# Kernel optimization log

Hardware: AMD Instinct MI355X
Metric: run time of the kernel (lower is better)

The kernel has to match this reference:

```python
import jax, jax.numpy as jnp
import numpy as np
from jax import lax

B, L, R = 128, 256, 36
D_TXT, D_IMG, D_SOC = 768, 2048, 10
EPS = 0.05 ** 2        # geomloss blur=0.05, p=2 -> epsilon = blur^p
N_ITERS = 20           # fixed log-domain Sinkhorn iterations
GAMMA = 0.01


def _pcost(x, y):
    # x: [B,n,d], y: [B,m,d] -> C_ij = ||x_i - y_j||^2 / 2 (geomloss p=2 cost)
    xx = jnp.sum(x * x, -1)[:, :, None]
    yy = jnp.sum(y * y, -1)[:, None, :]
    xy = jnp.einsum('bnd,bmd->bnm', x, y)
    return 0.5 * (xx + yy - 2.0 * xy)


def _sinkhorn_cost(C, loga, logb, eps, n_iters):
    # Log-domain Sinkhorn; masked points carry loga/logb = -inf (zero weight).
    f = jnp.zeros(loga.shape, C.dtype)
    g = jnp.zeros(logb.shape, C.dtype)

    def body(fg, _):
        f, g = fg
        g = -eps * jax.nn.logsumexp(loga[:, :, None] + (f[:, :, None] - C) / eps, axis=1)
        f = -eps * jax.nn.logsumexp(logb[:, None, :] + (g[:, None, :] - C) / eps, axis=2)
        return (f, g), None

    (f, g), _ = lax.scan(body, (f, g), None, length=n_iters)
    a = jnp.exp(loga)  # exp(-inf) = 0 for masked entries
    b = jnp.exp(logb)
    return jnp.sum(a * f, -1) + jnp.sum(b * g, -1)  # <a,f> + <b,g>


def _forward(txt_global, txt_region, img_global, img_region, social, attn_mask,
             W_stat, b_stat, W_gt, b_gt, W_gi, b_gi, W_rt, b_rt, W_ri, b_ri,
             W_m1, b_m1, W_m2, b_m2):
    relu = jax.nn.relu
    soc = relu(social @ W_stat + b_stat)                            # [B,100]
    tg = relu(jnp.concatenate([txt_global, soc], axis=1) @ W_gt + b_gt)  # [B,200]
    ig = relu(img_global @ W_gi + b_gi)                              # [B,200]
    h = relu((tg + ig) @ W_m1 + b_m1)
    mix_pred = h @ W_m2 + b_m2                                       # [B,2]

    tr = relu(txt_region @ W_rt + b_rt)                              # [B,L,50]
    ir = relu(img_region @ W_ri + b_ri)                              # [B,R,50]

    Bn, _, _ = tr.shape
    Rn = ir.shape[1]
    mask = attn_mask > 0
    n_words = jnp.sum(attn_mask, axis=-1).astype(tr.dtype)          # [B]
    loga = jnp.where(mask, -jnp.log(n_words)[:, None], -jnp.inf)    # uniform over valid tokens
    logb = jnp.full((Bn, Rn), -jnp.log(float(Rn)), tr.dtype)        # uniform over regions

    # Debiased Sinkhorn divergence (geomloss SamplesLoss default debias=True):
    Sxy = _sinkhorn_cost(_pcost(tr, ir), loga, logb, EPS, N_ITERS)
    Sxx = _sinkhorn_cost(_pcost(tr, tr), loga, loga, EPS, N_ITERS)
    Syy = _sinkhorn_cost(_pcost(ir, ir), logb, logb, EPS, N_ITERS)
    w_dis = Sxy - 0.5 * (Sxx + Syy)                                  # [B]

    w_pred = jnp.stack([1.0 - GAMMA * w_dis, GAMMA * w_dis], axis=1)  # [B,2]
    logit = jax.nn.softmax(jnp.maximum(mix_pred, w_pred), axis=1)
    return logit


def setup_inputs() -> dict:
    key = jax.random.key(0)
    ks = jax.random.split(key, 24)
    init = lambda k, s: (jax.random.normal(k, s) * 0.02).astype(jnp.float32)
    lengths = jax.random.randint(ks[0], (B,), 16, L + 1)             # ragged lengths
    attn_mask = (jnp.arange(L)[None, :] < lengths[:, None]).astype(jnp.int32)
    return {
        'txt_global': jax.random.normal(ks[1], (B, D_TXT), jnp.float32),
        'txt_region': jax.random.normal(ks[2], (B, L, D_TXT), jnp.float32),
        'img_global': jax.random.normal(ks[3], (B, D_IMG), jnp.float32),
        'img_region': jax.random.normal(ks[4], (B, R, D_IMG), jnp.float32),
        'social': jax.random.normal(ks[5], (B, D_SOC), jnp.float32),
        'attn_mask': attn_mask,
        'W_stat': init(ks[6], (D_SOC, 100)), 'b_stat': jnp.zeros((100,), jnp.float32),
        'W_gt': init(ks[7], (868, 200)), 'b_gt': jnp.zeros((200,), jnp.float32),
        'W_gi': init(ks[8], (D_IMG, 200)), 'b_gi': jnp.zeros((200,), jnp.float32),
        'W_rt': init(ks[9], (D_TXT, 50)), 'b_rt': jnp.zeros((50,), jnp.float32),
        'W_ri': init(ks[10], (D_IMG, 50)), 'b_ri': jnp.zeros((50,), jnp.float32),
        'W_m1': init(ks[11], (200, 100)), 'b_m1': jnp.zeros((100,), jnp.float32),
        'W_m2': init(ks[12], (100, 2)), 'b_m2': jnp.zeros((2,), jnp.float32),
    }


def reference(txt_global, txt_region, img_global, img_region, social, attn_mask,
              W_stat, b_stat, W_gt, b_gt, W_gi, b_gi, W_rt, b_rt, W_ri, b_ri,
              W_m1, b_m1, W_m2, b_m2):
    return _forward(txt_global, txt_region, img_global, img_region, social, attn_mask,
                    W_stat, b_stat, W_gt, b_gt, W_gi, b_gi, W_rt, b_rt, W_ri, b_ri,
                    W_m1, b_m1, W_m2, b_m2)
```

## Files before the change

kernel.cpp:

```cpp
#include <hip/hip_runtime.h>

typedef float  f32x4 __attribute__((ext_vector_type(4)));
typedef short  s16x8 __attribute__((ext_vector_type(8)));

#define EPS_LN2      0.0017328679513998632f
#define INV_EPS_LN2  577.0780163555852f
#define LOG2_36      5.169925001442312f

__device__ __forceinline__ short f2bf(float x) {
  unsigned int u; __builtin_memcpy(&u, &x, 4);
  u = (u + 0x7FFFu + ((u >> 16) & 1u)) >> 16;
  return (short)u;
}

__global__ __launch_bounds__(256) void k_pack(const float* __restrict__ W_rt,
                                              const float* __restrict__ W_ri,
                                              short* __restrict__ frt,
                                              short* __restrict__ fri,
                                              float* __restrict__ pre1,
                                              float* __restrict__ pre2) {
  int slot = blockIdx.x * 256 + threadIdx.x;
  for (int z = slot; z < 25600; z += 22528) { pre1[z] = 0.f; pre2[z] = 0.f; }
  const float* W; short* dst; int f;
  if (slot < 6144) { W = W_rt; dst = frt; f = slot; }
  else             { W = W_ri; dst = fri; f = slot - 6144; }
  int k32 = f >> 8, rem = f & 255, ct = rem >> 6, l = rem & 63;
  int col = ct * 16 + (l & 15);
  int k0  = k32 * 32 + (l >> 4) * 8;
  s16x8 p;
#pragma unroll
  for (int c = 0; c < 8; ++c) {
    float v = (col < 50) ? W[(k0 + c) * 50 + col] : 0.f;
    p[c] = f2bf(v);
  }
  *(s16x8*)(dst + (long)f * 8) = p;
}

__global__ __launch_bounds__(256) void k_gemm(
    const float* __restrict__ txt, const float* __restrict__ img,
    const float* __restrict__ social,
    const float* __restrict__ W_stat, const float* __restrict__ b_stat,
    const float* __restrict__ W_gt, const float* __restrict__ W_gi,
    float* __restrict__ pre1, float* __restrict__ pre2) {
  __shared__ float sA[32][128];
  int bid = blockIdx.x;
  int job = bid >> 4, rb = (bid >> 2) & 3, cb = bid & 3;
  int t = threadIdx.x, r0 = rb * 32;
  const float* W; float* dst; int k0, klen;
  if (job < 6)       { k0 = job * 128;     klen = 128; W = W_gt;             dst = pre1; }
  else if (job == 6) { k0 = 0;             klen = 100; W = W_gt + 768 * 200; dst = pre1; }
  else               { k0 = (job - 7)*128; klen = 128; W = W_gi;             dst = pre2; }
  if (job == 6) {
    for (int idx = t; idx < 4096; idx += 256) {
      int r = idx >> 7, k = idx & 127;
      float v = 0.f;
      if (k < 100) {
        v = b_stat[k];
#pragma unroll
        for (int u = 0; u < 10; ++u) v += social[(r0 + r) * 10 + u] * W_stat[u * 100 + k];
        v = fmaxf(v, 0.f);
      }
      sA[r][k] = v;
    }
  } else {
    const float* A = (job < 6) ? txt : img;
    int K_A = (job < 6) ? 768 : 2048;
    for (int idx = t; idx < 4096; idx += 256) {
      int r = idx >> 7, k = idx & 127;
      sA[r][k] = A[(r0 + r) * K_A + k0 + k];
    }
  }
  __syncthreads();
  int c = cb * 64 + (t & 63), rg = t >> 6;
  if (c < 200) {
    float acc[8];
#pragma unroll
    for (int i = 0; i < 8; ++i) acc[i] = 0.f;
    for (int k4 = 0; k4 < klen; k4 += 4) {
      float w0 = W[(k0 + k4    ) * 200 + c];
      float w1 = W[(k0 + k4 + 1) * 200 + c];
      float w2 = W[(k0 + k4 + 2) * 200 + c];
      float w3 = W[(k0 + k4 + 3) * 200 + c];
#pragma unroll
      for (int i = 0; i < 8; ++i) {
        f32x4 a = *(const f32x4*)&sA[rg * 8 + i][k4];
        acc[i] += a[0]*w0 + a[1]*w1 + a[2]*w2 + a[3]*w3;
      }
    }
#pragma unroll
    for (int i = 0; i < 8; ++i)
      atomicAdd(&dst[(r0 + rg * 8 + i) * 200 + c], acc[i]);
  }
}

template<int K32>
__device__ __forceinline__ void proj_body(const float* __restrict__ A,
                                          const short* __restrict__ Bf,
                                          const float* __restrict__ bias,
                                          float* __restrict__ out, int bid) {
  int wave = threadIdx.x >> 6, lane = threadIdx.x & 63;
  int tile = bid * 4 + wave;
  int row0 = tile * 16;
  int rl = lane & 15, q = lane >> 4;
  const int K = K32 * 32;
  const float* ar = A + (long)(row0 + rl) * K + q * 8;
  f32x4 acc[4];
#pragma unroll
  for (int ct = 0; ct < 4; ++ct) acc[ct] = (f32x4){0.f, 0.f, 0.f, 0.f};
  for (int k32 = 0; k32 < K32; ++k32) {
    f32x4 a0 = *(const f32x4*)(ar + k32 * 32);
    f32x4 a1 = *(const f32x4*)(ar + k32 * 32 + 4);
    s16x8 af;
    af[0]=f2bf(a0[0]); af[1]=f2bf(a0[1]); af[2]=f2bf(a0[2]); af[3]=f2bf(a0[3]);
    af[4]=f2bf(a1[0]); af[5]=f2bf(a1[1]); af[6]=f2bf(a1[2]); af[7]=f2bf(a1[3]);
    const short* bp = Bf + (long)(k32 * 4) * 512 + lane * 8;
#pragma unroll
    for (int ct = 0; ct < 4; ++ct) {
      s16x8 bfr = *(const s16x8*)(bp + ct * 512);
      acc[ct] = __builtin_amdgcn_mfma_f32_16x16x32_bf16(af, bfr, acc[ct], 0, 0, 0);
    }
  }
#pragma unroll
  for (int ct = 0; ct < 4; ++ct) {
    int col = ct * 16 + rl;
    float bv = (col < 50) ? bias[col] : 0.f;
#pragma unroll
    for (int r = 0; r < 4; ++r) {
      int grow = row0 + q * 4 + r;
      float o = fmaxf(acc[ct][r] + bv, 0.f);
      out[(long)grow * 64 + col] = (col < 50) ? o : 0.f;
    }
  }
}

__device__ __forceinline__ void mix_body(
    int r, const float* __restrict__ pre1, const float* __restrict__ pre2,
    const float* __restrict__ b_gt, const float* __restrict__ b_gi,
    const float* __restrict__ W_m1, const float* __restrict__ b_m1,
    const float* __restrict__ W_m2, const float* __restrict__ b_m2,
    float* __restrict__ mix) {
  __shared__ float sm[200];
  __shared__ float sh[100];
  int t = threadIdx.x;
  if (t < 200)
    sm[t] = fmaxf(pre1[r * 200 + t] + b_gt[t], 0.f) +
            fmaxf(pre2[r * 200 + t] + b_gi[t], 0.f);
  __syncthreads();
  if (t < 100) {
    float a = b_m1[t];
#pragma unroll 4
    for (int k = 0; k < 200; ++k) a += sm[k] * W_m1[k * 100 + t];
    sh[t] = fmaxf(a, 0.f);
  }
  __syncthreads();
  if (t < 2) {
    float a = b_m2[t];
    for (int k = 0; k < 100; ++k) a += sh[k] * W_m2[k * 2 + t];
    mix[r * 2 + t] = a;
  }
}

__global__ __launch_bounds__(256) void k_pm(
    const float* __restrict__ txt_region, const short* __restrict__ frt,
    const float* __restrict__ b_rt, float* __restrict__ tr,
    const float* __restrict__ img_region, const short* __restrict__ fri,
    const float* __restrict__ b_ri, float* __restrict__ ir,
    const float* __restrict__ pre1, const float* __restrict__ pre2,
    const float* __restrict__ b_gt, const float* __restrict__ b_gi,
    const float* __restrict__ W_m1, const float* __restrict__ b_m1,
    const float* __restrict__ W_m2, const float* __restrict__ b_m2,
    float* __restrict__ mix) {
  int bid = blockIdx.x;
  if (bid < 512)      proj_body<24>(txt_region, frt, b_rt, tr, bid);
  else if (bid < 584) proj_body<64>(img_region, fri, b_ri, ir, bid - 512);
  else mix_body(bid - 584, pre1, pre2, b_gt, b_gi, W_m1, b_m1, W_m2, b_m2, mix);
}

#define SK_SMEM 50736

__global__ __launch_bounds__(1024)
__attribute__((amdgpu_waves_per_eu(4, 4)))
void k_sink(
    const float* __restrict__ tr, const float* __restrict__ ir,
    const int* __restrict__ amask, float* __restrict__ Cxx,
    float* __restrict__ Sxy, float* __restrict__ Sxx, float* __restrict__ Syy) {
  __shared__ __align__(16) char smem[SK_SMEM];
  int role = blockIdx.x >> 7;
  int b    = blockIdx.x & 127;
  int tid  = threadIdx.x;

  if (role == 0) {
    short* Xf    = (short*)smem;
    float* norms = (float*)(smem + 32768);
    float* sA    = (float*)(smem + 33792);
    float* sF    = (float*)(smem + 34816);
    float* sG    = (float*)(smem + 35840);
    float* sPm   = (float*)(smem + 36864);
    int*   nsh   = (int*)  (smem + 40960);
    if (tid < 64) {
      int c = 0;
      for (int i = tid; i < 256; i += 64) c += amask[b * 256 + i];
#pragma unroll
      for (int o = 1; o < 64; o <<= 1) c += __shfl_xor(c, o);
      if (tid == 0) *nsh = c;
    }
    const float* Xg = tr + (long)b * 256 * 64;
    for (int slot = tid; slot < 2048; slot += 1024) {
      int t = slot >> 7, k32 = (slot >> 6) & 1, l = slot & 63;
      int row = t * 16 + (l & 15), k0 = k32 * 32 + (l >> 4) * 8;
      const float* src = Xg + row * 64 + k0;
      f32x4 a0 = *(const f32x4*)src, a1 = *(const f32x4*)(src + 4);
      s16x8 p;
      p[0]=f2bf(a0[0]); p[1]=f2bf(a0[1]); p[2]=f2bf(a0[2]); p[3]=f2bf(a0[3]);
      p[4]=f2bf(a1[0]); p[5]=f2bf(a1[1]); p[6]=f2bf(a1[2]); p[7]=f2bf(a1[3]);
      *(s16x8*)(Xf + slot * 8) = p;
    }
    __syncthreads();
    int n = *nsh;
    int wv = tid >> 6, lane = tid & 63, q = lane >> 4;
    f32x4 acc[16];
#pragma unroll
    for (int ct = 0; ct < 16; ++ct) acc[ct] = (f32x4){0.f, 0.f, 0.f, 0.f};
    s16x8 afr0 = *(const s16x8*)(Xf + ((wv * 2 + 0) * 64 + lane) * 8);
    s16x8 afr1 = *(const s16x8*)(Xf + ((wv * 2 + 1) * 64 + lane) * 8);
#pragma unroll
    for (int ct = 0; ct < 16; ++ct) {
      s16x8 b0 = *(const s16x8*)(Xf + ((ct * 2 + 0) * 64 + lane) * 8);
      s16x8 b1 = *(const s16x8*)(Xf + ((ct * 2 + 1) * 64 + lane) * 8);
      acc[ct] = __builtin_amdgcn_mfma_f32_16x16x32_bf16(afr0, b0, acc[ct], 0, 0, 0);
      acc[ct] = __builtin_amdgcn_mfma_f32_16x16x32_bf16(afr1, b1, acc[ct], 0, 0, 0);
    }
#pragma unroll
    for (int r = 0; r < 4; ++r) {
      int m_ = q * 4 + r;
      if ((lane & 15) == m_) norms[wv * 16 + m_] = acc[wv][r];
    }
    __syncthreads();
    float* Cwb = Cxx + (long)b * 65536;
    if (wv * 16 < n) {
#pragma unroll
      for (int ct = 0; ct < 16; ++ct) {
        int gj = ct * 16 + (lane & 15);
        float nj = norms[gj];
#pragma unroll
        for (int r = 0; r < 4; ++r) {
          int gi = wv * 16 + q * 4 + r;
          Cwb[gi * 256 + gj] = (acc[ct][r] - 0.5f * (norms[gi] + nj)) * INV_EPS_LN2;
        }
      }
    }
    __syncthreads();
    int kk = tid >> 8, j = tid & 255, i0 = kk * 64;
    int iend = n - i0; if (iend > 64) iend = 64;
    float Creg[64];
    if (j < n) {
#pragma unroll
      for (int ch = 0; ch < 4; ++ch) {
        if (ch * 16 < iend) {
#pragma unroll
          for (int u = 0; u < 16; ++u)
            Creg[ch * 16 + u] = Cwb[(i0 + ch * 16 + u) * 256 + j];
        }
      }
    }
    float log2n = log2f((float)n);
    if (tid < 256) { sF[tid] = 0.f; sA[tid] = (tid < n) ? -log2n : -1e30f; }
    __syncthreads();
    const float* ap = sA + i0;
    for (int h = 0; h < 40; ++h) {
      float m = -1e30f;
      if (j < n) {
#pragma unroll
        for (int ch = 0; ch < 4; ++ch) {
          if (ch * 16 < iend) {
            f32x4 a0 = *(const f32x4*)(ap + ch * 16);
            f32x4 a1 = *(const f32x4*)(ap + ch * 16 + 4);
            f32x4 a2 = *(const f32x4*)(ap + ch * 16 + 8);
            f32x4 a3 = *(const f32x4*)(ap + ch * 16 + 12);
            float t0 = fmaxf(a0[0] + Creg[ch*16+0],  a0[1] + Creg[ch*16+1]);
            float t1 = fmaxf(a0[2] + Creg[ch*16+2],  a0[3] + Creg[ch*16+3]);
            float t2 = fmaxf(a1[0] + Creg[ch*16+4],  a1[1] + Creg[ch*16+5]);
            float t3 = fmaxf(a1[2] + Creg[ch*16+6],  a1[3] + Creg[ch*16+7]);
            float t4 = fmaxf(a2[0] + Creg[ch*16+8],  a2[1] + Creg[ch*16+9]);
            float t5 = fmaxf(a2[2] + Creg[ch*16+10], a2[3] + Creg[ch*16+11]);
            float t6 = fmaxf(a3[0] + Creg[ch*16+12], a3[1] + Creg[ch*16+13]);
            float t7 = fmaxf(a3[2] + Creg[ch*16+14], a3[3] + Creg[ch*16+15]);
            float u0 = fmaxf(fmaxf(t0, t1), fmaxf(t2, t3));
            float u1 = fmaxf(fmaxf(t4, t5), fmaxf(t6, t7));
            m = fmaxf(m, fmaxf(u0, u1));
          }
        }
      }
      sPm[kk * 256 + j] = m;
      __syncthreads();
      if (tid < 256) {
        float m4 = fmaxf(fmaxf(sPm[tid], sPm[256 + tid]),
                         fmaxf(sPm[512 + tid], sPm[768 + tid]));
        if (tid < n) {
          ((h & 1) ? sF : sG)[tid] = -EPS_LN2 * m4;
          sA[tid] = -log2n - m4;
        }
      }
      __syncthreads();
    }
    if (tid < 64) {
      float a = 0.f;
      for (int i = tid; i < n; i += 64) a += sF[i] + sG[i];
#pragma unroll
      for (int o = 1; o < 64; o <<= 1) a += __shfl_xor(a, o);
      if (tid == 0) Sxx[b] = a / n;
    }
  } else if (role == 1) {
    float* Ys  = (float*)smem;
    float* Cs  = (float*)(smem + 9216);
    float* nx  = (float*)(smem + 47104);
    float* ny  = (float*)(smem + 48128);
    float* sA  = (float*)(smem + 48288);
    float* sB  = (float*)(smem + 49376);
    float* sF  = (float*)(smem + 49536);
    float* sG  = (float*)(smem + 50560);
    int*   nsh = (int*)  (smem + 50720);
    if (tid < 64) {
      int c = 0;
      for (int i = tid; i < 256; i += 64) c += amask[b * 256 + i];
#pragma unroll
      for (int o = 1; o < 64; o <<= 1) c += __shfl_xor(c, o);
      if (tid == 0) *nsh = c;
    }
    const float* Xg = tr + (long)b * 256 * 64;
    const float* Yg = ir + (long)b * 36 * 64;
    for (int idx = tid; idx < 576; idx += 1024) {
      int row = idx >> 4, q4 = idx & 15;
      *(f32x4*)(Ys + row * 64 + q4 * 4) = *(const f32x4*)(Yg + row * 64 + q4 * 4);
    }
    __syncthreads();
    int n = *nsh;
    if (tid < 256) {
      float a = 0.f;
#pragma unroll
      for (int q4 = 0; q4 < 13; ++q4) {
        f32x4 v = *(const f32x4*)(Xg + tid * 64 + q4 * 4);
        a += v[0]*v[0] + v[1]*v[1] + v[2]*v[2] + v[3]*v[3];
      }
      nx[tid] = a;
    } else if (tid < 292) {
      int jj = tid - 256; float a = 0.f;
#pragma unroll
      for (int q4 = 0; q4 < 13; ++q4) {
        f32x4 v = *(const f32x4*)(Ys + jj * 64 + q4 * 4);
        a += v[0]*v[0] + v[1]*v[1] + v[2]*v[2] + v[3]*v[3];
      }
      ny[jj] = a;
    }
    __syncthreads();
    if (tid < 1008) {
      int ii = tid / 36, jj = tid - ii * 36;
      f32x4 yr[13];
#pragma unroll
      for (int q4 = 0; q4 < 13; ++q4) yr[q4] = *(const f32x4*)(Ys + jj * 64 + q4 * 4);
      float nyj = ny[jj];
      for (int i = ii; i < 256; i += 28) {
        float d = 0.f;
#pragma unroll
        for (int q4 = 0; q4 < 13; ++q4) {
          f32x4 xv = *(const f32x4*)(Xg + i * 64 + q4 * 4);
          d += xv[0]*yr[q4][0] + xv[1]*yr[q4][1] + xv[2]*yr[q4][2] + xv[3]*yr[q4][3];
        }
        Cs[i * 37 + jj] = (d - 0.5f * (nx[i] + nyj)) * INV_EPS_LN2;
      }
    }
    __syncthreads();
    int jg = tid >> 4, kg = tid & 15;
    float Cg[16];
    if (jg < 36) {
#pragma unroll
      for (int t = 0; t < 16; ++t) Cg[t] = Cs[(kg * 16 + t) * 37 + jg];
    }
    int fi = tid >> 2, kf = tid & 3;
    float Cf[9];
#pragma unroll
    for (int t = 0; t < 9; ++t) {
      int jj2 = kf * 9 + t;
      Cf[t] = (jj2 < 36) ? Cs[fi * 37 + jj2] : 0.f;
    }
    float log2n = log2f((float)n);
    if (tid < 256) { sF[tid] = 0.f; sA[tid + (tid >> 4)] = -log2n; }
    __syncthreads();
    const float* agp = sA + kg * 17;
    int gend = n - kg * 16; if (gend > 16) gend = 16;
    for (int it = 0; it < 20; ++it) {
      float gm = -1e30f;
      if (jg < 36) {
#pragma unroll
        for (int t = 0; t < 16; ++t)
          if (t < gend) gm = fmaxf(gm, agp[t] + Cg[t]);
        gm = fmaxf(gm, __shfl_xor(gm, 1)); gm = fmaxf(gm, __shfl_xor(gm, 2));
        gm = fmaxf(gm, __shfl_xor(gm, 4)); gm = fmaxf(gm, __shfl_xor(gm, 8));
      }
      __syncthreads();
      if (jg < 36 && kg == 0) {
        sG[jg] = -EPS_LN2 * gm;
        sB[jg] = -LOG2_36 - gm;
      }
      __syncthreads();
      float fm = -1e30f;
#pragma unroll
      for (int t = 0; t < 9; ++t) {
        int jj2 = kf * 9 + t;
        if (jj2 < 36) fm = fmaxf(fm, sB[jj2] + Cf[t]);
      }
      fm = fmaxf(fm, __shfl_xor(fm, 1)); fm = fmaxf(fm, __shfl_xor(fm, 2));
      __syncthreads();
      if (kf == 0 && fi < n) {
        sF[fi] = -EPS_LN2 * fm;
        sA[fi + (fi >> 4)] = -log2n - fm;
      }
      __syncthreads();
    }
    if (tid < 64) {
      float a = 0.f;
      for (int i = tid; i < n; i += 64) a += sF[i];
      float g = (tid < 36) ? sG[tid] : 0.f;
#pragma unroll
      for (int o = 1; o < 64; o <<= 1) { a += __shfl_xor(a, o); g += __shfl_xor(g, o); }
      if (tid == 0) Sxy[b] = a / n + g / 36.f;
    }
  } else {
    float* Ys = (float*)smem;
    float* Cs = (float*)(smem + 9216);
    float* ny = (float*)(smem + 48128);
    float* sA = (float*)(smem + 48288);
    float* sF = (float*)(smem + 49536);
    float* sG = (float*)(smem + 50560);
    const float* Yg = ir + (long)b * 36 * 64;
    for (int idx = tid; idx < 576; idx += 1024) {
      int row = idx >> 4, q4 = idx & 15;
      *(f32x4*)(Ys + row * 64 + q4 * 4) = *(const f32x4*)(Yg + row * 64 + q4 * 4);
    }
    __syncthreads();
    if (tid < 36) {
      float a = 0.f;
#pragma unroll
      for (int q4 = 0; q4 < 13; ++q4) {
        f32x4 v = *(const f32x4*)(Ys + tid * 64 + q4 * 4);
        a += v[0]*v[0] + v[1]*v[1] + v[2]*v[2] + v[3]*v[3];
      }
      ny[tid] = a;
    }
    __syncthreads();
    if (tid < 1008) {
      int ii = tid / 36, jj = tid - ii * 36;
      f32x4 yr[13];
#pragma unroll
      for (int q4 = 0; q4 < 13; ++q4) yr[q4] = *(const f32x4*)(Ys + jj * 64 + q4 * 4);
      float nyj = ny[jj];
      for (int i = ii; i < 36; i += 28) {
        float d = 0.f;
#pragma unroll
        for (int q4 = 0; q4 < 13; ++q4) {
          f32x4 xv = *(const f32x4*)(Ys + i * 64 + q4 * 4);
          d += xv[0]*yr[q4][0] + xv[1]*yr[q4][1] + xv[2]*yr[q4][2] + xv[3]*yr[q4][3];
        }
        Cs[i * 37 + jj] = (d - 0.5f * (ny[i] + nyj)) * INV_EPS_LN2;
      }
    }
    __syncthreads();
    int j = tid >> 2, kk = tid & 3;
    float Creg[9];
    if (j < 36) {
#pragma unroll
      for (int t = 0; t < 9; ++t) {
        int i2 = kk * 9 + t;
        Creg[t] = (i2 < 36) ? Cs[i2 * 37 + j] : 0.f;
      }
    }
    if (tid < 36) { sF[tid] = 0.f; sA[tid] = -LOG2_36; }
    __syncthreads();
    for (int h = 0; h < 40; ++h) {
      float m = -1e30f;
      if (j < 36) {
#pragma unroll
        for (int t = 0; t < 9; ++t) {
          int i2 = kk * 9 + t;
          if (i2 < 36) m = fmaxf(m, sA[i2] + Creg[t]);
        }
        m = fmaxf(m, __shfl_xor(m, 1)); m = fmaxf(m, __shfl_xor(m, 2));
      }
      __syncthreads();
      if (j < 36 && kk == 0) {
        ((h & 1) ? sF : sG)[j] = -EPS_LN2 * m;
        sA[j] = -LOG2_36 - m;
      }
      __syncthreads();
    }
    if (tid < 64) {
      float a = (tid < 36) ? sF[tid] + sG[tid] : 0.f;
#pragma unroll
      for (int o = 1; o < 64; o <<= 1) a += __shfl_xor(a, o);
      if (tid == 0) Syy[b] = a / 36.f;
    }
  }
}

__global__ void k_final(const float* __restrict__ mix, const float* __restrict__ sxy,
                        const float* __restrict__ sxx, const float* __restrict__ syy,
                        float* __restrict__ out) {
  int b = blockIdx.x * 64 + threadIdx.x;
  if (b < 128) {
    float w  = sxy[b] - 0.5f * (sxx[b] + syy[b]);
    float x0 = fmaxf(mix[b * 2 + 0], 1.0f - 0.01f * w);
    float x1 = fmaxf(mix[b * 2 + 1], 0.01f * w);
    float mx = fmaxf(x0, x1);
    float e0 = expf(x0 - mx), e1 = expf(x1 - mx);
    float inv = 1.f / (e0 + e1);
    out[b * 2 + 0] = e0 * inv;
    out[b * 2 + 1] = e1 * inv;
  }
}

extern "C" void kernel_launch(void* const* d_in, const int* in_sizes, int n_in,
                              void* d_out, int out_size, void* d_ws, size_t ws_size,
                              hipStream_t stream) {
  const float* txt_global = (const float*)d_in[0];
  const float* txt_region = (const float*)d_in[1];
  const float* img_global = (const float*)d_in[2];
  const float* img_region = (const float*)d_in[3];
  const float* social     = (const float*)d_in[4];
  const int*   attn_mask  = (const int*)  d_in[5];
  const float* W_stat = (const float*)d_in[6];  const float* b_stat = (const float*)d_in[7];
  const float* W_gt   = (const float*)d_in[8];  const float* b_gt   = (const float*)d_in[9];
  const float* W_gi   = (const float*)d_in[10]; const float* b_gi   = (const float*)d_in[11];
  const float* W_rt   = (const float*)d_in[12]; const float* b_rt   = (const float*)d_in[13];
  const float* W_ri   = (const float*)d_in[14]; const float* b_ri   = (const float*)d_in[15];
  const float* W_m1   = (const float*)d_in[16]; const float* b_m1   = (const float*)d_in[17];
  const float* W_m2   = (const float*)d_in[18]; const float* b_m2   = (const float*)d_in[19];

  float* ws = (float*)d_ws;
  float* ws_mix = ws;
  float* ws_sxy = ws + 256;
  float* ws_sxx = ws + 384;
  float* ws_syy = ws + 512;
  short* ws_frt = (short*)(ws + 1024);
  short* ws_fri = (short*)(ws + 25600);
  float* ws_pre1 = ws + 103936;
  float* ws_tr  = ws + 131072;
  float* ws_ir  = ws + 2228224;
  float* ws_cxx = ws + 2523136;
  float* ws_pre2 = ws_cxx;

  k_pack<<<88, 256, 0, stream>>>(W_rt, W_ri, ws_frt, ws_fri, ws_pre1, ws_pre2);
  k_gemm<<<368, 256, 0, stream>>>(txt_global, img_global, social,
                                  W_stat, b_stat, W_gt, W_gi, ws_pre1, ws_pre2);
  k_pm<<<712, 256, 0, stream>>>(txt_region, ws_frt, b_rt, ws_tr,
                                img_region, ws_fri, b_ri, ws_ir,
                                ws_pre1, ws_pre2, b_gt, b_gi,
                                W_m1, b_m1, W_m2, b_m2, ws_mix);
  k_sink<<<384, 1024, 0, stream>>>(ws_tr, ws_ir, attn_mask, ws_cxx,
                                   ws_sxy, ws_sxx, ws_syy);
  k_final<<<2, 64, 0, stream>>>(ws_mix, ws_sxy, ws_sxx, ws_syy, (float*)d_out);
}
```

Measured before the change: 347.6 us.

## Merge pack and global GEMM kernels, stage projection weights in LDS with prefetch

Folds the weight-packing kernel into the global GEMM kernel, which removes one launch. The GEMM now writes per-job partial sums to separate buffers instead of using atomics, so the buffers no longer need zeroing and the mix stage sums the 23 partials itself. The region-projection body double-buffers the packed bf16 weights through 64KB of shared memory and prefetches the next A fragment in registers, so the waves of a block share one weight read from global memory. The Sinkhorn max-reduction is reshaped into 3-input fmax trees. The larger LDS allocation limits blocks per CU and adds barriers in the projection loop.

```diff
diff --git a/kernel.cpp b/kernel.cpp
--- a/kernel.cpp
+++ b/kernel.cpp
@@ -13,43 +13,40 @@
   return (short)u;
 }
 
-__global__ __launch_bounds__(256) void k_pack(const float* __restrict__ W_rt,
-                                              const float* __restrict__ W_ri,
-                                              short* __restrict__ frt,
-                                              short* __restrict__ fri,
-                                              float* __restrict__ pre1,
-                                              float* __restrict__ pre2) {
-  int slot = blockIdx.x * 256 + threadIdx.x;
-  for (int z = slot; z < 25600; z += 22528) { pre1[z] = 0.f; pre2[z] = 0.f; }
-  const float* W; short* dst; int f;
-  if (slot < 6144) { W = W_rt; dst = frt; f = slot; }
-  else             { W = W_ri; dst = fri; f = slot - 6144; }
-  int k32 = f >> 8, rem = f & 255, ct = rem >> 6, l = rem & 63;
-  int col = ct * 16 + (l & 15);
-  int k0  = k32 * 32 + (l >> 4) * 8;
-  s16x8 p;
-#pragma unroll
-  for (int c = 0; c < 8; ++c) {
-    float v = (col < 50) ? W[(k0 + c) * 50 + col] : 0.f;
-    p[c] = f2bf(v);
-  }
-  *(s16x8*)(dst + (long)f * 8) = p;
-}
-
-__global__ __launch_bounds__(256) void k_gemm(
+__global__ __launch_bounds__(256) void k_prep(
+    const float* __restrict__ W_rt, const float* __restrict__ W_ri,
+    short* __restrict__ frt, short* __restrict__ fri,
     const float* __restrict__ txt, const float* __restrict__ img,
     const float* __restrict__ social,
     const float* __restrict__ W_stat, const float* __restrict__ b_stat,
     const float* __restrict__ W_gt, const float* __restrict__ W_gi,
-    float* __restrict__ pre1, float* __restrict__ pre2) {
+    float* __restrict__ pre) {
   __shared__ float sA[32][128];
   int bid = blockIdx.x;
-  int job = bid >> 4, rb = (bid >> 2) & 3, cb = bid & 3;
+  if (bid < 88) {
+    int slot = bid * 256 + threadIdx.x;
+    const float* W; short* dst; int f;
+    if (slot < 6144) { W = W_rt; dst = frt; f = slot; }
+    else             { W = W_ri; dst = fri; f = slot - 6144; }
+    int k32 = f >> 8, rem = f & 255, ct = rem >> 6, l = rem & 63;
+    int col = ct * 16 + (l & 15);
+    int k0  = k32 * 32 + (l >> 4) * 8;
+    s16x8 p;
+#pragma unroll
+    for (int c = 0; c < 8; ++c) {
+      float v = (col < 50) ? W[(k0 + c) * 50 + col] : 0.f;
+      p[c] = f2bf(v);
+    }
+    *(s16x8*)(dst + (long)f * 8) = p;
+    return;
+  }
+  int gb = bid - 88;
+  int job = gb >> 4, rb = (gb >> 2) & 3, cb = gb & 3;
   int t = threadIdx.x, r0 = rb * 32;
-  const float* W; float* dst; int k0, klen;
-  if (job < 6)       { k0 = job * 128;     klen = 128; W = W_gt;             dst = pre1; }
-  else if (job == 6) { k0 = 0;             klen = 100; W = W_gt + 768 * 200; dst = pre1; }
-  else               { k0 = (job - 7)*128; klen = 128; W = W_gi;             dst = pre2; }
+  const float* W; int k0, klen;
+  if (job < 6)       { k0 = job * 128;       klen = 128; W = W_gt; }
+  else if (job == 6) { k0 = 0;               klen = 100; W = W_gt + 768 * 200; }
+  else               { k0 = (job - 7) * 128; klen = 128; W = W_gi; }
   if (job == 6) {
     for (int idx = t; idx < 4096; idx += 256) {
       int r = idx >> 7, k = idx & 127;
@@ -87,9 +84,10 @@
         acc[i] += a[0]*w0 + a[1]*w1 + a[2]*w2 + a[3]*w3;
       }
     }
+    float* dst = pre + (long)job * 25600;
 #pragma unroll
     for (int i = 0; i < 8; ++i)
-      atomicAdd(&dst[(r0 + rg * 8 + i) * 200 + c], acc[i]);
+      dst[(r0 + rg * 8 + i) * 200 + c] = acc[i];
   }
 }
 
@@ -97,27 +95,63 @@
 __device__ __forceinline__ void proj_body(const float* __restrict__ A,
                                           const short* __restrict__ Bf,
                                           const float* __restrict__ bias,
-                                          float* __restrict__ out, int bid) {
+                                          float* __restrict__ out, int bid,
+                                          char* smem) {
+  short* sB = (short*)smem;
+  const int NWIN = K32 / 8;
   int wave = threadIdx.x >> 6, lane = threadIdx.x & 63;
-  int tile = bid * 4 + wave;
-  int row0 = tile * 16;
   int rl = lane & 15, q = lane >> 4;
+  int row0 = bid * 64 + wave * 16;
   const int K = K32 * 32;
   const float* ar = A + (long)(row0 + rl) * K + q * 8;
+  int soff = wave * 4096 + lane * 8;
+
+  f32x4 stage[8];
+#pragma unroll
+  for (int c = 0; c < 8; ++c)
+    stage[c] = *(const f32x4*)(Bf + (long)soff + c * 512);
+#pragma unroll
+  for (int c = 0; c < 8; ++c)
+    *(f32x4*)(sB + soff + c * 512) = stage[c];
+  f32x4 a0 = *(const f32x4*)(ar);
+  f32x4 a1 = *(const f32x4*)(ar + 4);
   f32x4 acc[4];
 #pragma unroll
   for (int ct = 0; ct < 4; ++ct) acc[ct] = (f32x4){0.f, 0.f, 0.f, 0.f};
-  for (int k32 = 0; k32 < K32; ++k32) {
-    f32x4 a0 = *(const f32x4*)(ar + k32 * 32);
-    f32x4 a1 = *(const f32x4*)(ar + k32 * 32 + 4);
-    s16x8 af;
-    af[0]=f2bf(a0[0]); af[1]=f2bf(a0[1]); af[2]=f2bf(a0[2]); af[3]=f2bf(a0[3]);
-    af[4]=f2bf(a1[0]); af[5]=f2bf(a1[1]); af[6]=f2bf(a1[2]); af[7]=f2bf(a1[3]);
-    const short* bp = Bf + (long)(k32 * 4) * 512 + lane * 8;
-#pragma unroll
-    for (int ct = 0; ct < 4; ++ct) {
-      s16x8 bfr = *(const s16x8*)(bp + ct * 512);
-      acc[ct] = __builtin_amdgcn_mfma_f32_16x16x32_bf16(af, bfr, acc[ct], 0, 0, 0);
+  __syncthreads();
+
+  for (int w = 0; w < NWIN; ++w) {
+    if (w + 1 < NWIN) {
+      const short* src = Bf + (long)(w + 1) * 16384 + soff;
+#pragma unroll
+      for (int c = 0; c < 8; ++c) stage[c] = *(const f32x4*)(src + c * 512);
+    }
+    const short* bbuf = sB + (w & 1) * 16384;
+#pragma unroll
+    for (int kk8 = 0; kk8 < 8; ++kk8) {
+      int k32 = w * 8 + kk8;
+      f32x4 na0, na1;
+      if (k32 + 1 < K32) {
+        na0 = *(const f32x4*)(ar + (k32 + 1) * 32);
+        na1 = *(const f32x4*)(ar + (k32 + 1) * 32 + 4);
+      }
+      s16x8 af;
+      af[0]=f2bf(a0[0]); af[1]=f2bf(a0[1]); af[2]=f2bf(a0[2]); af[3]=f2bf(a0[3]);
+      af[4]=f2bf(a1[0]); af[5]=f2bf(a1[1]); af[6]=f2bf(a1[2]); af[7]=f2bf(a1[3]);
+      const short* bp = bbuf + kk8 * 2048 + lane * 8;
+#pragma unroll
+      for (int ct = 0; ct < 4; ++ct) {
+        s16x8 bfr = *(const s16x8*)(bp + ct * 512);
+        acc[ct] = __builtin_amdgcn_mfma_f32_16x16x32_bf16(af, bfr, acc[ct], 0, 0, 0);
+      }
+      a0 = na0; a1 = na1;
+    }
+    if (w + 1 < NWIN) {
+      __syncthreads();
+      short* nbuf = sB + ((w + 1) & 1) * 16384;
+#pragma unroll
+      for (int c = 0; c < 8; ++c) *(f32x4*)(nbuf + soff + c * 512) = stage[c];
+      __syncthreads();
     }
   }
 #pragma unroll
@@ -134,17 +168,22 @@
 }
 
 __device__ __forceinline__ void mix_body(
-    int r, const float* __restrict__ pre1, const float* __restrict__ pre2,
+    int r, const float* __restrict__ pre,
     const float* __restrict__ b_gt, const float* __restrict__ b_gi,
     const float* __restrict__ W_m1, const float* __restrict__ b_m1,
     const float* __restrict__ W_m2, const float* __restrict__ b_m2,
-    float* __restrict__ mix) {
-  __shared__ float sm[200];
-  __shared__ float sh[100];
+    float* __restrict__ mix, char* smem) {
+  float* sm = (float*)smem;
+  float* sh = (float*)(smem + 800);
   int t = threadIdx.x;
-  if (t < 200)
-    sm[t] = fmaxf(pre1[r * 200 + t] + b_gt[t], 0.f) +
-            fmaxf(pre2[r * 200 + t] + b_gi[t], 0.f);
+  if (t < 200) {
+    float s1 = b_gt[t], s2 = b_gi[t];
+#pragma unroll
+    for (int j = 0; j < 7; ++j)  s1 += pre[(long)j * 25600 + r * 200 + t];
+#pragma unroll
+    for (int j = 7; j < 23; ++j) s2 += pre[(long)j * 25600 + r * 200 + t];
+    sm[t] = fmaxf(s1, 0.f) + fmaxf(s2, 0.f);
+  }
   __syncthreads();
   if (t < 100) {
     float a = b_m1[t];
@@ -160,20 +199,23 @@
   }
 }
 
-__global__ __launch_bounds__(256) void k_pm(
+__global__ __launch_bounds__(256)
+__attribute__((amdgpu_waves_per_eu(4, 4)))
+void k_pm(
     const float* __restrict__ txt_region, const short* __restrict__ frt,
     const float* __restrict__ b_rt, float* __restrict__ tr,
     const float* __restrict__ img_region, const short* __restrict__ fri,
     const float* __restrict__ b_ri, float* __restrict__ ir,
-    const float* __restrict__ pre1, const float* __restrict__ pre2,
+    const float* __restrict__ pre,
     const float* __restrict__ b_gt, const float* __restrict__ b_gi,
     const float* __restrict__ W_m1, const float* __restrict__ b_m1,
     const float* __restrict__ W_m2, const float* __restrict__ b_m2,
     float* __restrict__ mix) {
+  __shared__ __align__(16) char smem[65536];
   int bid = blockIdx.x;
-  if (bid < 512)      proj_body<24>(txt_region, frt, b_rt, tr, bid);
-  else if (bid < 584) proj_body<64>(img_region, fri, b_ri, ir, bid - 512);
-  else mix_body(bid - 584, pre1, pre2, b_gt, b_gi, W_m1, b_m1, W_m2, b_m2, mix);
+  if (bid < 128)      mix_body(bid, pre, b_gt, b_gi, W_m1, b_m1, W_m2, b_m2, mix, smem);
+  else if (bid < 640) proj_body<24>(txt_region, frt, b_rt, tr, bid - 128, smem);
+  else                proj_body<64>(img_region, fri, b_ri, ir, bid - 640, smem);
 }
 
 #define SK_SMEM 50736
@@ -273,21 +315,27 @@
 #pragma unroll
         for (int ch = 0; ch < 4; ++ch) {
           if (ch * 16 < iend) {
-            f32x4 a0 = *(const f32x4*)(ap + ch * 16);
-            f32x4 a1 = *(const f32x4*)(ap + ch * 16 + 4);
-            f32x4 a2 = *(const f32x4*)(ap + ch * 16 + 8);
-            f32x4 a3 = *(const f32x4*)(ap + ch * 16 + 12);
-            float t0 = fmaxf(a0[0] + Creg[ch*16+0],  a0[1] + Creg[ch*16+1]);
-            float t1 = fmaxf(a0[2] + Creg[ch*16+2],  a0[3] + Creg[ch*16+3]);
-            float t2 = fmaxf(a1[0] + Creg[ch*16+4],  a1[1] + Creg[ch*16+5]);
-            float t3 = fmaxf(a1[2] + Creg[ch*16+6],  a1[3] + Creg[ch*16+7]);
-            float t4 = fmaxf(a2[0] + Creg[ch*16+8],  a2[1] + Creg[ch*16+9]);
-            float t5 = fmaxf(a2[2] + Creg[ch*16+10], a2[3] + Creg[ch*16+11]);
-            float t6 = fmaxf(a3[0] + Creg[ch*16+12], a3[1] + Creg[ch*16+13]);
-            float t7 = fmaxf(a3[2] + Creg[ch*16+14], a3[3] + Creg[ch*16+15]);
-            float u0 = fmaxf(fmaxf(t0, t1), fmaxf(t2, t3));
-            float u1 = fmaxf(fmaxf(t4, t5), fmaxf(t6, t7));
-            m = fmaxf(m, fmaxf(u0, u1));
+            const float* app = ap + ch * 16;
+            f32x4 A0 = *(const f32x4*)(app);
+            f32x4 A1 = *(const f32x4*)(app + 4);
+            f32x4 A2 = *(const f32x4*)(app + 8);
+            f32x4 A3 = *(const f32x4*)(app + 12);
+            float x0 = A0[0]+Creg[ch*16+0],  x1 = A0[1]+Creg[ch*16+1];
+            float x2 = A0[2]+Creg[ch*16+2],  x3 = A0[3]+Creg[ch*16+3];
+            float x4 = A1[0]+Creg[ch*16+4],  x5 = A1[1]+Creg[ch*16+5];
+            float x6 = A1[2]+Creg[ch*16+6],  x7 = A1[3]+Creg[ch*16+7];
+            float x8 = A2[0]+Creg[ch*16+8],  x9 = A2[1]+Creg[ch*16+9];
+            float xa = A2[2]+Creg[ch*16+10], xb = A2[3]+Creg[ch*16+11];
+            float xc = A3[0]+Creg[ch*16+12], xd = A3[1]+Creg[ch*16+13];
+            float xe = A3[2]+Creg[ch*16+14], xf = A3[3]+Creg[ch*16+15];
+            float y0 = fmaxf(fmaxf(x0, x1), x2);
+            float y1 = fmaxf(fmaxf(x3, x4), x5);
+            float y2 = fmaxf(fmaxf(x6, x7), x8);
+            float y3 = fmaxf(fmaxf(x9, xa), xb);
+            float y4 = fmaxf(fmaxf(xc, xd), xe);
+            float z0 = fmaxf(fmaxf(y0, y1), y2);
+            float z1 = fmaxf(fmaxf(y3, y4), xf);
+            m = fmaxf(fmaxf(m, z0), z1);
           }
         }
       }
@@ -542,18 +590,17 @@
   float* ws_syy = ws + 512;
   short* ws_frt = (short*)(ws + 1024);
   short* ws_fri = (short*)(ws + 25600);
-  float* ws_pre1 = ws + 103936;
   float* ws_tr  = ws + 131072;
   float* ws_ir  = ws + 2228224;
   float* ws_cxx = ws + 2523136;
-  float* ws_pre2 = ws_cxx;
-
-  k_pack<<<88, 256, 0, stream>>>(W_rt, W_ri, ws_frt, ws_fri, ws_pre1, ws_pre2);
-  k_gemm<<<368, 256, 0, stream>>>(txt_global, img_global, social,
-                                  W_stat, b_stat, W_gt, W_gi, ws_pre1, ws_pre2);
+  float* ws_pre = ws_cxx;
+
+  k_prep<<<456, 256, 0, stream>>>(W_rt, W_ri, ws_frt, ws_fri,
+                                  txt_global, img_global, social,
+                                  W_stat, b_stat, W_gt, W_gi, ws_pre);
   k_pm<<<712, 256, 0, stream>>>(txt_region, ws_frt, b_rt, ws_tr,
                                 img_region, ws_fri, b_ri, ws_ir,
-                                ws_pre1, ws_pre2, b_gt, b_gi,
+                                ws_pre, b_gt, b_gi,
                                 W_m1, b_m1, W_m2, b_m2, ws_mix);
   k_sink<<<384, 1024, 0, stream>>>(ws_tr, ws_ir, attn_mask, ws_cxx,
                                    ws_sxy, ws_sxx, ws_syy);
```

Result: no change. 340.8 us (-2.0%).
